# Performance work log

Measured on AMD Instinct MI355X. Metric: run time of the kernel, lower is better.

## Reference

```python
import jax, jax.numpy as jnp
import numpy as np

NP_, NA, NPR = 3000, 25, 1071
N = NP_ + NA + NPR          # 4096 total nodes
D = 256                     # latent_dim
H = 8                       # num_heads
DH = D // H                 # head dim 32
FF = 4 * D                  # feed-forward dim
BLOCKS = 3                  # args.block_num
E = 131072                  # edges = N * 32 avg degree
EPS = 1e-5


def setup_inputs() -> dict:
    key = jax.random.key(0)
    ks = jax.random.split(key, 16)
    s = 1.0 / np.sqrt(D)
    return {
        "adj_row": jax.random.randint(ks[0], (E,), 0, N, dtype=jnp.int32),
        "adj_col": jax.random.randint(ks[1], (E,), 0, N, dtype=jnp.int32),
        "adj_val": jax.random.uniform(ks[2], (E,), dtype=jnp.float32),
        "pe": jax.random.normal(ks[3], (NP_, D), dtype=jnp.float32) * s,
        "ae": jax.random.normal(ks[4], (NA, D), dtype=jnp.float32) * s,
        "qe": jax.random.normal(ks[5], (NPR, D), dtype=jnp.float32) * s,
        "Wqkv": jax.random.normal(ks[6], (D, 3 * D), dtype=jnp.float32) * s,
        "Wo": jax.random.normal(ks[7], (D, D), dtype=jnp.float32) * s,
        "W1": jax.random.normal(ks[8], (D, FF), dtype=jnp.float32) * s,
        "b1": jnp.zeros((FF,), dtype=jnp.float32),
        "W2": jax.random.normal(ks[9], (FF, D), dtype=jnp.float32) * (1.0 / np.sqrt(FF)),
        "b2": jnp.zeros((D,), dtype=jnp.float32),
        "ln1_g": jnp.ones((D,), dtype=jnp.float32),
        "ln1_b": jnp.zeros((D,), dtype=jnp.float32),
        "ln2_g": jnp.ones((D,), dtype=jnp.float32),
        "ln2_b": jnp.zeros((D,), dtype=jnp.float32),
    }


def _layer_norm(x, g, b):
    m = jnp.mean(x, axis=-1, keepdims=True)
    v = jnp.mean(jnp.square(x - m), axis=-1, keepdims=True)
    return (x - m) * jax.lax.rsqrt(v + EPS) * g + b


def _encoder_layer(x, Wqkv, Wo, W1, b1, W2, b2, ln1_g, ln1_b, ln2_g, ln2_b):
    # x: [N, D]; standard post-LN transformer encoder (dropout = 0)
    qkv = x @ Wqkv                                   # [N, 3D]
    q, k, v = jnp.split(qkv, 3, axis=-1)
    q = q.reshape(N, H, DH)
    k = k.reshape(N, H, DH)
    v = v.reshape(N, H, DH)
    scores = jnp.einsum("nhd,mhd->hnm", q, k) / np.sqrt(DH)  # [H, N, N]
    att = jax.nn.softmax(scores, axis=-1)
    o = jnp.einsum("hnm,mhd->nhd", att, v).reshape(N, D) @ Wo
    x = _layer_norm(x + o, ln1_g, ln1_b)
    h = jax.nn.relu(x @ W1 + b1) @ W2 + b2
    return _layer_norm(x + h, ln2_g, ln2_b)


def _spmm(adj_row, adj_col, adj_val, x):
    # sparse [N,N] @ dense [N,D] via gather + segment-sum scatter
    msgs = adj_val[:, None] * x[adj_col]             # [E, D]
    return jax.ops.segment_sum(msgs, adj_row, num_segments=N)


def reference(adj_row, adj_col, adj_val, pe, ae, qe, Wqkv, Wo, W1, b1, W2, b2,
              ln1_g, ln1_b, ln2_g, ln2_b):
    cur = jnp.concatenate([pe, ae, qe], axis=0)      # [N, D]
    total = cur
    for _ in range(BLOCKS):
        t = _spmm(adj_row, adj_col, adj_val, cur)
        t = _encoder_layer(t, Wqkv, Wo, W1, b1, W2, b2, ln1_g, ln1_b, ln2_g, ln2_b)
        cur = t + cur                                # residual per block
        total = total + cur                          # sum over embeds list
    protein = total[:NP_]
    aa = total[NP_:NP_ + NA]
    prop = total[NP_ + NA:]
    return total, protein, aa, prop
```

## Files before the change

### kernel.cpp

```cpp
#include <hip/hip_runtime.h>
#include <hip/hip_bf16.h>


#define NPROT 3000
#define NAA   25
#define NPROP 1071
#define NTOT  4096
#define DIM   256
#define NH    8
#define DHD   32
#define FFD   1024
#define NEDGE 131072
#define LNEPS 1e-5f
#define KSPLIT 4
#define KVQ (NTOT/KSPLIT)

typedef unsigned short u16;
typedef unsigned int u32;
typedef __attribute__((ext_vector_type(8))) short short8v;
typedef __attribute__((ext_vector_type(4))) float float4v;
typedef __attribute__((ext_vector_type(2))) unsigned int uint2v;

__device__ __forceinline__ u16 f2bu(float x){
  union { __hip_bfloat16 h; u16 u; } c; c.h = __float2bfloat16(x); return c.u;
}
__device__ __forceinline__ float bu2f(u16 u){
  union { u32 i; float f; } c; c.i = ((u32)u) << 16; return c.f;
}
__device__ __forceinline__ float4v mfma16(short8v a, short8v b, float4v c){
  return __builtin_amdgcn_mfma_f32_16x16x32_bf16(a, b, c, 0, 0, 0);
}
__device__ __forceinline__ u32 packbf(float lo, float hi){
  u32 ul = __builtin_bit_cast(u32, lo);
  u32 uh = __builtin_bit_cast(u32, hi);
  return (ul >> 16) | (uh & 0xFFFF0000u);
}

__global__ __launch_bounds__(256) void k_embed(const float* __restrict__ pe, const float* __restrict__ ae,
                                               const float* __restrict__ qe,
                                               float* __restrict__ cur, float* __restrict__ tot){
  int i = blockIdx.x*256 + threadIdx.x;
  int row = i >> 8;
  float v;
  if (row < NPROT)           v = pe[i];
  else if (row < NPROT+NAA)  v = ae[i - NPROT*DIM];
  else                       v = qe[i - (NPROT+NAA)*DIM];
  cur[i] = v; tot[i] = v;
}

__global__ __launch_bounds__(256) void k_zero(int* __restrict__ p, int n){
  int i = blockIdx.x*256 + threadIdx.x; if (i < n) p[i] = 0;
}

__global__ __launch_bounds__(256) void k_wconv(const float* __restrict__ W, u16* __restrict__ Wt,
                                               int K, int N){
  int n = blockIdx.x;
  for (int k = threadIdx.x; k < K; k += 256)
    Wt[(size_t)n*K + k] = f2bu(W[(size_t)k*N + n]);
}

__global__ __launch_bounds__(256) void k_hist(const int* __restrict__ rows, int* __restrict__ cnt){
  int e = blockIdx.x*256 + threadIdx.x; if (e < NEDGE) atomicAdd(&cnt[rows[e]], 1);
}

__global__ __launch_bounds__(64) void k_scan(const int* __restrict__ cnt, int* __restrict__ rowptr,
                                             int* __restrict__ cursor){
  int lane = threadIdx.x;
  int sum = 0;
  for (int i = 0; i < 64; ++i) sum += cnt[lane*64 + i];
  int pref = sum;
  #pragma unroll
  for (int off = 1; off < 64; off <<= 1){
    int u = __shfl_up(pref, off);
    if (lane >= off) pref += u;
  }
  int run = pref - sum;
  for (int i = 0; i < 64; ++i){
    int c = cnt[lane*64 + i];
    rowptr[lane*64 + i] = run;
    cursor[lane*64 + i] = run;
    run += c;
  }
  if (lane == 63) rowptr[NTOT] = run;
}

__global__ __launch_bounds__(256) void k_scatter(const int* __restrict__ rows, const int* __restrict__ cols,
                                                 const float* __restrict__ vals, int* __restrict__ cursor,
                                                 int* __restrict__ ccol, float* __restrict__ cval){
  int e = blockIdx.x*256 + threadIdx.x; if (e >= NEDGE) return;
  int p = atomicAdd(&cursor[rows[e]], 1);
  ccol[p] = cols[e]; cval[p] = vals[e];
}

__global__ __launch_bounds__(256) void k_spmm(const int* __restrict__ rowptr, const int* __restrict__ ccol,
                                              const float* __restrict__ cval, const float* __restrict__ x,
                                              float* __restrict__ out, u16* __restrict__ outb){
  int r = blockIdx.x, c = threadIdx.x;
  int s = rowptr[r], e = rowptr[r+1];
  float acc = 0.f;
  for (int i = s; i < e; ++i)
    acc += cval[i] * x[((size_t)ccol[i] << 8) + c];
  out[((size_t)r << 8) + c] = acc;
  outb[((size_t)r << 8) + c] = f2bu(acc);
}

template<int RELU, int BIAS, int BF16OUT>
__global__ __launch_bounds__(256) void k_gemm64(const u16* __restrict__ A, const u16* __restrict__ Wt,
                                                const float* __restrict__ bias, void* __restrict__ Cv,
                                                int M, int K, int Nc){
  __shared__ u16 Al[64*64];
  __shared__ u16 Bl[64*64];
  const int tid = threadIdx.x;
  const int w  = tid >> 6, l = tid & 63, lr = l & 15, g = l >> 4;
  const int row0 = blockIdx.y*64, col0 = blockIdx.x*64;
  const int wm = (w >> 1)*32, wn = (w & 1)*32;
  const int sm = tid >> 2;
  const int so = (tid & 3)*2;
  float4v acc[2][2] = {};

  for (int k0 = 0; k0 < K; k0 += 64){
    const u16* As = A  + (size_t)(row0 + sm)*K + k0 + so*8;
    const u16* Bs = Wt + (size_t)(col0 + sm)*K + k0 + so*8;
    #pragma unroll
    for (int j = 0; j < 2; ++j){
      int o = so + j;
      int slot = o ^ (sm & 7);
      *(short8v*)(Al + sm*64 + slot*8) = *(const short8v*)(As + j*8);
      *(short8v*)(Bl + sm*64 + slot*8) = *(const short8v*)(Bs + j*8);
    }
    __syncthreads();
    #pragma unroll
    for (int kk = 0; kk < 2; ++kk){
      short8v af[2], bfr[2];
      #pragma unroll
      for (int i = 0; i < 2; ++i){
        int am = wm + 16*i + lr;
        af[i]  = *(const short8v*)(Al + am*64 + (((4*kk + g) ^ (am & 7))*8));
        int bn = wn + 16*i + lr;
        bfr[i] = *(const short8v*)(Bl + bn*64 + (((4*kk + g) ^ (bn & 7))*8));
      }
      acc[0][0] = mfma16(af[0], bfr[0], acc[0][0]);
      acc[0][1] = mfma16(af[0], bfr[1], acc[0][1]);
      acc[1][0] = mfma16(af[1], bfr[0], acc[1][0]);
      acc[1][1] = mfma16(af[1], bfr[1], acc[1][1]);
    }
    __syncthreads();
  }

  #pragma unroll
  for (int mi = 0; mi < 2; ++mi){
    #pragma unroll
    for (int ni = 0; ni < 2; ++ni){
      int col = col0 + wn + 16*ni + lr;
      float bv = BIAS ? bias[col] : 0.f;
      #pragma unroll
      for (int j = 0; j < 4; ++j){
        int row = row0 + wm + 16*mi + 4*g + j;
        float v = acc[mi][ni][j] + bv;
        if (RELU) v = fmaxf(v, 0.f);
        if (BF16OUT) ((u16*)Cv)[(size_t)row*Nc + col] = f2bu(v);
        else         ((float*)Cv)[(size_t)row*Nc + col] = v;
      }
    }
  }
}

__global__ __launch_bounds__(256) void k_attn_mfma(const u16* __restrict__ qbf,
                                                   u16* __restrict__ op,
                                                   float* __restrict__ mbuf, float* __restrict__ lbuf){
  __shared__ u16 Vt[2][32*64];
  __shared__ u16 Pl[4][16*64];
  __shared__ float Fl[4][16];
  const int h   = blockIdx.y;
  const int ks  = blockIdx.z;
  const int qb  = blockIdx.x * 64;
  const int tid = threadIdx.x;
  const int w   = tid >> 6;
  const int l   = tid & 63;
  const int lr  = l & 15;
  const int g   = l >> 4;
  const int sr  = tid >> 2;
  const int sq  = tid & 3;
  const float SC  = 0.17677669529663687f;
  const float SCL = 0.25503837f;
  u16* opart = op + (size_t)ks*NTOT*DIM;

  short8v qf = *(const short8v*)(qbf + (size_t)(qb + 16*w + lr)*768 + h*DHD + 8*g);
  short8v ones;
  #pragma unroll
  for (int j = 0; j < 8; ++j) ones[j] = (short)0x3F80;

  float4v oa0 = {0.f,0.f,0.f,0.f}, oa1 = {0.f,0.f,0.f,0.f};
  float4v accl = {0.f,0.f,0.f,0.f};
  float mrun = -1e30f;
  u16* pw = &Pl[w][0];

  const u16* vp = qbf + (size_t)(ks*KVQ + sr)*768 + 512 + h*DHD + 8*sq;
  const u16* kp = qbf + (size_t)(ks*KVQ + lr)*768 + 256 + h*DHD + 8*g;
  short8v vreg = *(const short8v*)vp;
  short8v kf0 = *(const short8v*)(kp);
  short8v kf1 = *(const short8v*)(kp + (size_t)16*768);
  short8v kf2 = *(const short8v*)(kp + (size_t)32*768);
  short8v kf3 = *(const short8v*)(kp + (size_t)48*768);

  const int NIT = KVQ/64;
  for (int t = 0; t < NIT; ++t){
    u16* vt = &Vt[t & 1][0];
    #pragma unroll
    for (int j = 0; j < 8; ++j){
      int row  = 8*sq + j;
      int slot = (sr >> 3) ^ j;
      vt[row*64 + slot*8 + (sr & 7)] = (u16)vreg[j];
    }
    __syncthreads();
    vp += (size_t)64*768;
    if (t + 1 < NIT) vreg = *(const short8v*)vp;

    float4v s0 = mfma16(kf0, qf, (float4v){0.f,0.f,0.f,0.f});
    float4v s1 = mfma16(kf1, qf, (float4v){0.f,0.f,0.f,0.f});
    float4v s2 = mfma16(kf2, qf, (float4v){0.f,0.f,0.f,0.f});
    float4v s3 = mfma16(kf3, qf, (float4v){0.f,0.f,0.f,0.f});
    if (t + 1 < NIT){
      const u16* kn = kp + (size_t)(t+1)*64*768;
      kf0 = *(const short8v*)(kn);
      kf1 = *(const short8v*)(kn + (size_t)16*768);
      kf2 = *(const short8v*)(kn + (size_t)32*768);
      kf3 = *(const short8v*)(kn + (size_t)48*768);
    }

    float m0 = fmaxf(fmaxf(fmaxf(s0[0],s0[1]),s0[2]),s0[3]);
    float m1 = fmaxf(fmaxf(fmaxf(s1[0],s1[1]),s1[2]),s1[3]);
    float m2 = fmaxf(fmaxf(fmaxf(s2[0],s2[1]),s2[2]),s2[3]);
    float m3 = fmaxf(fmaxf(fmaxf(s3[0],s3[1]),s3[2]),s3[3]);
    float tm = fmaxf(fmaxf(fmaxf(m0,m1),m2),m3);
    tm = fmaxf(tm, __shfl_xor(tm, 16));
    tm = fmaxf(tm, __shfl_xor(tm, 32));
    const bool nomax = __all(tm <= mrun);
    float fac = 1.f;
    if (!nomax){
      float mn = fmaxf(mrun, tm);
      fac = exp2f((mrun - mn)*SCL);
      mrun = mn;
    }
    float mns = mrun*SCL;
    #pragma unroll
    for (int j = 0; j < 4; ++j){
      s0[j] = exp2f(__builtin_fmaf(s0[j], SCL, -mns));
      s1[j] = exp2f(__builtin_fmaf(s1[j], SCL, -mns));
      s2[j] = exp2f(__builtin_fmaf(s2[j], SCL, -mns));
      s3[j] = exp2f(__builtin_fmaf(s3[j], SCL, -mns));
    }

    {
      int gh = g >> 1, gl = 4*(g & 1);
      uint2v* d0 = (uint2v*)(pw + lr*64 + ((0 + gh) ^ (lr & 7))*8 + gl);
      uint2v* d1 = (uint2v*)(pw + lr*64 + ((2 + gh) ^ (lr & 7))*8 + gl);
      uint2v* d2 = (uint2v*)(pw + lr*64 + ((4 + gh) ^ (lr & 7))*8 + gl);
      uint2v* d3 = (uint2v*)(pw + lr*64 + ((6 + gh) ^ (lr & 7))*8 + gl);
      *d0 = (uint2v){packbf(s0[0],s0[1]), packbf(s0[2],s0[3])};
      *d1 = (uint2v){packbf(s1[0],s1[1]), packbf(s1[2],s1[3])};
      *d2 = (uint2v){packbf(s2[0],s2[1]), packbf(s2[2],s2[3])};
      *d3 = (uint2v){packbf(s3[0],s3[1]), packbf(s3[2],s3[3])};
    }

    if (!nomax){
      if (g == 0) Fl[w][lr] = fac;
      float fq0 = Fl[w][4*g+0], fq1 = Fl[w][4*g+1], fq2 = Fl[w][4*g+2], fq3 = Fl[w][4*g+3];
      oa0[0]*=fq0; oa0[1]*=fq1; oa0[2]*=fq2; oa0[3]*=fq3;
      oa1[0]*=fq0; oa1[1]*=fq1; oa1[2]*=fq2; oa1[3]*=fq3;
      accl[0]*=fq0; accl[1]*=fq1; accl[2]*=fq2; accl[3]*=fq3;
    }

    #pragma unroll
    for (int kk = 0; kk < 2; ++kk){
      int slotp = (4*kk + g) ^ (lr & 7);
      short8v pa = *(const short8v*)(pw + lr*64 + slotp*8);
      short8v v0 = *(const short8v*)(vt + lr*64        + slotp*8);
      short8v v1 = *(const short8v*)(vt + (lr+16)*64   + slotp*8);
      oa0  = mfma16(pa, v0, oa0);
      oa1  = mfma16(pa, v1, oa1);
      accl = mfma16(pa, ones, accl);
    }
  }

  #pragma unroll
  for (int j = 0; j < 4; ++j){
    size_t row = (size_t)(qb + 16*w + 4*g + j);
    opart[row*DIM + h*DHD + lr]      = f2bu(oa0[j]);
    opart[row*DIM + h*DHD + 16 + lr] = f2bu(oa1[j]);
  }
  if (l < 16){
    size_t mi = (size_t)(ks*NH + h)*NTOT + qb + 16*w + lr;
    mbuf[mi] = mrun*SC;
  }
  if (lr == 0){
    #pragma unroll
    for (int j = 0; j < 4; ++j){
      size_t mi = (size_t)(ks*NH + h)*NTOT + qb + 16*w + 4*g + j;
      lbuf[mi] = accl[j];
    }
  }
}

__global__ __launch_bounds__(256) void k_attn_merge(const u16* __restrict__ op,
                                                    const float* __restrict__ mbuf, const float* __restrict__ lbuf,
                                                    u16* __restrict__ obf){
  int i = blockIdx.x*256 + threadIdx.x;
  int r = i >> 8, c = i & 255, h = c >> 5;
  float m[KSPLIT], wgt[KSPLIT];
  float M = -1e30f;
  #pragma unroll
  for (int k = 0; k < KSPLIT; ++k){
    m[k] = mbuf[(size_t)(k*NH + h)*NTOT + r];
    M = fmaxf(M, m[k]);
  }
  float L = 0.f, acc = 0.f;
  #pragma unroll
  for (int k = 0; k < KSPLIT; ++k){
    wgt[k] = __expf(m[k] - M);
    L   += wgt[k]*lbuf[(size_t)(k*NH + h)*NTOT + r];
    acc += wgt[k]*bu2f(op[(size_t)k*NTOT*DIM + i]);
  }
  obf[i] = f2bu(acc / L);
}

template<int DUAL>
__global__ __launch_bounds__(256) void k_add_ln(const float* __restrict__ a, const float* __restrict__ b,
                                                const float* __restrict__ g, const float* __restrict__ be,
                                                float* __restrict__ out, u16* __restrict__ out2){
  __shared__ float red[4];
  int r = blockIdx.x, c = threadIdx.x;
  float v = a[((size_t)r << 8) + c] + b[((size_t)r << 8) + c];
  float s = v;
  #pragma unroll
  for (int off = 32; off; off >>= 1) s += __shfl_down(s, off);
  if ((c & 63) == 0) red[c >> 6] = s;
  __syncthreads();
  float mean = (red[0]+red[1]+red[2]+red[3]) * (1.f/DIM);
  __syncthreads();
  float d = v - mean;
  float s2 = d*d;
  #pragma unroll
  for (int off = 32; off; off >>= 1) s2 += __shfl_down(s2, off);
  if ((c & 63) == 0) red[c >> 6] = s2;
  __syncthreads();
  float var = (red[0]+red[1]+red[2]+red[3]) * (1.f/DIM);
  float rv = d * rsqrtf(var + LNEPS) * g[c] + be[c];
  out[((size_t)r << 8) + c] = rv;
  if (DUAL) out2[((size_t)r << 8) + c] = f2bu(rv);
}

__global__ __launch_bounds__(256) void k_add_ln_upd(const float* __restrict__ a, const float* __restrict__ b,
                                                    const float* __restrict__ g, const float* __restrict__ be,
                                                    float* __restrict__ cur, float* __restrict__ tot){
  __shared__ float red[4];
  int r = blockIdx.x, c = threadIdx.x;
  size_t idx = ((size_t)r << 8) + c;
  float v = a[idx] + b[idx];
  float s = v;
  #pragma unroll
  for (int off = 32; off; off >>= 1) s += __shfl_down(s, off);
  if ((c & 63) == 0) red[c >> 6] = s;
  __syncthreads();
  float mean = (red[0]+red[1]+red[2]+red[3]) * (1.f/DIM);
  __syncthreads();
  float d = v - mean;
  float s2 = d*d;
  #pragma unroll
  for (int off = 32; off; off >>= 1) s2 += __shfl_down(s2, off);
  if ((c & 63) == 0) red[c >> 6] = s2;
  __syncthreads();
  float var = (red[0]+red[1]+red[2]+red[3]) * (1.f/DIM);
  float rv = d * rsqrtf(var + LNEPS) * g[c] + be[c];
  float cu = cur[idx] + rv;
  cur[idx] = cu;
  tot[idx] += cu;
}

__global__ __launch_bounds__(256) void k_out(const float* __restrict__ tot, float* __restrict__ out){
  int i = blockIdx.x*256 + threadIdx.x;
  float v = tot[i];
  out[i] = v;
  out[NTOT*DIM + i] = v;
}

extern "C" void kernel_launch(void* const* d_in, const int* in_sizes, int n_in,
                              void* d_out, int out_size, void* d_ws, size_t ws_size,
                              hipStream_t stream){
  const int*   adj_row = (const int*)  d_in[0];
  const int*   adj_col = (const int*)  d_in[1];
  const float* adj_val = (const float*)d_in[2];
  const float* pe   = (const float*)d_in[3];
  const float* ae   = (const float*)d_in[4];
  const float* qe   = (const float*)d_in[5];
  const float* Wqkv = (const float*)d_in[6];
  const float* Wo   = (const float*)d_in[7];
  const float* W1   = (const float*)d_in[8];
  const float* b1   = (const float*)d_in[9];
  const float* W2   = (const float*)d_in[10];
  const float* b2   = (const float*)d_in[11];
  const float* g1   = (const float*)d_in[12];
  const float* be1  = (const float*)d_in[13];
  const float* g2   = (const float*)d_in[14];
  const float* be2  = (const float*)d_in[15];
  float* out = (float*)d_out;

  char* w = (char*)d_ws;
  float* cur  = (float*)w; w += (size_t)NTOT*DIM*4;
  float* tot  = (float*)w; w += (size_t)NTOT*DIM*4;
  float* tf   = (float*)w; w += (size_t)NTOT*DIM*4;
  float* pbuf = (float*)w; w += (size_t)NTOT*DIM*4;
  float* x1   = (float*)w; w += (size_t)NTOT*DIM*4;
  u16* tbf    = (u16*)w;   w += (size_t)NTOT*DIM*2;
  u16* obf    = (u16*)w;   w += (size_t)NTOT*DIM*2;
  u16* x1b    = (u16*)w;   w += (size_t)NTOT*DIM*2;
  u16* hq     = (u16*)w;   w += (size_t)NTOT*FFD*2;
  u16* wqkvt  = (u16*)w;   w += (size_t)768*256*2;
  u16* wot    = (u16*)w;   w += (size_t)256*256*2;
  u16* w1t    = (u16*)w;   w += (size_t)1024*256*2;
  u16* w2t    = (u16*)w;   w += (size_t)256*1024*2;
  int* rowptr = (int*)w;   w += (size_t)(NTOT+1)*4;
  int* cnt    = (int*)w;   w += (size_t)NTOT*4;
  int* cursor = (int*)w;   w += (size_t)NTOT*4;
  int* ccol   = (int*)w;   w += (size_t)NEDGE*4;
  float* cval = (float*)w; w += (size_t)NEDGE*4;
  u16* qbf  = hq;
  u16* opbf = (u16*)pbuf;
  float* mbuf = (float*)tbf;
  float* lbuf = mbuf + (size_t)KSPLIT*NH*NTOT;

  k_zero<<<16, 256, 0, stream>>>(cnt, NTOT);
  k_embed<<<NTOT, 256, 0, stream>>>(pe, ae, qe, cur, tot);
  k_hist<<<NEDGE/256, 256, 0, stream>>>(adj_row, cnt);
  k_scan<<<1, 64, 0, stream>>>(cnt, rowptr, cursor);
  k_scatter<<<NEDGE/256, 256, 0, stream>>>(adj_row, adj_col, adj_val, cursor, ccol, cval);
  k_wconv<<<768,  256, 0, stream>>>(Wqkv, wqkvt, 256, 768);
  k_wconv<<<256,  256, 0, stream>>>(Wo,   wot,   256, 256);
  k_wconv<<<1024, 256, 0, stream>>>(W1,   w1t,   256, 1024);
  k_wconv<<<256,  256, 0, stream>>>(W2,   w2t,  1024, 256);

  for (int blk = 0; blk < 3; ++blk){
    k_spmm<<<NTOT, 256, 0, stream>>>(rowptr, ccol, cval, cur, tf, tbf);
    k_gemm64<0,0,1><<<dim3(768/64, NTOT/64), 256, 0, stream>>>(tbf, wqkvt, nullptr, qbf, NTOT, 256, 768);
    k_attn_mfma<<<dim3(NTOT/64, NH, KSPLIT), 256, 0, stream>>>(qbf, opbf, mbuf, lbuf);
    k_attn_merge<<<NTOT*DIM/256, 256, 0, stream>>>(opbf, mbuf, lbuf, obf);
    k_gemm64<0,0,0><<<dim3(256/64, NTOT/64), 256, 0, stream>>>(obf, wot, nullptr, pbuf, NTOT, 256, 256);
    k_add_ln<1><<<NTOT, 256, 0, stream>>>(tf, pbuf, g1, be1, x1, x1b);
    k_gemm64<1,1,1><<<dim3(1024/64, NTOT/64), 256, 0, stream>>>(x1b, w1t, b1, hq, NTOT, 256, 1024);
    k_gemm64<0,1,0><<<dim3(256/64, NTOT/64), 256, 0, stream>>>(hq, w2t, b2, pbuf, NTOT, 1024, 256);
    k_add_ln_upd<<<NTOT, 256, 0, stream>>>(x1, pbuf, g2, be2, cur, tot);
  }
  k_out<<<NTOT, 256, 0, stream>>>(tot, out);
}
```

Before: 492.5 us.

## Process 128 keys per attention iteration and halve the KV split

The flash-attention kernel now consumes 128 keys per loop iteration: eight K fragments, two transposed V tiles and a 128-wide P tile. The KV split drops from 4 to 2, so fewer partial outputs have to be combined afterwards. The rescale factor is broadcast with wave shuffles instead of a shared-memory round trip. The aim is fewer barriers and loop overheads and more MFMA/exp work per iteration, at the cost of more registers and half as many blocks. The prefetch of the next K/V tile is now unconditional, so the last iteration reads past the end of the slice.

```diff
diff --git a/kernel.cpp b/kernel.cpp
--- a/kernel.cpp
+++ b/kernel.cpp
@@ -12,7 +12,7 @@
 #define FFD   1024
 #define NEDGE 131072
 #define LNEPS 1e-5f
-#define KSPLIT 4
+#define KSPLIT 2
 #define KVQ (NTOT/KSPLIT)
 
 typedef unsigned short u16;
@@ -168,9 +168,8 @@
 __global__ __launch_bounds__(256) void k_attn_mfma(const u16* __restrict__ qbf,
                                                    u16* __restrict__ op,
                                                    float* __restrict__ mbuf, float* __restrict__ lbuf){
-  __shared__ u16 Vt[2][32*64];
-  __shared__ u16 Pl[4][16*64];
-  __shared__ float Fl[4][16];
+  __shared__ u16 Vt[2][2][32*64];
+  __shared__ u16 Pl[4][16*128];
   const int h   = blockIdx.y;
   const int ks  = blockIdx.z;
   const int qb  = blockIdx.x * 64;
@@ -197,42 +196,42 @@
 
   const u16* vp = qbf + (size_t)(ks*KVQ + sr)*768 + 512 + h*DHD + 8*sq;
   const u16* kp = qbf + (size_t)(ks*KVQ + lr)*768 + 256 + h*DHD + 8*g;
-  short8v vreg = *(const short8v*)vp;
-  short8v kf0 = *(const short8v*)(kp);
-  short8v kf1 = *(const short8v*)(kp + (size_t)16*768);
-  short8v kf2 = *(const short8v*)(kp + (size_t)32*768);
-  short8v kf3 = *(const short8v*)(kp + (size_t)48*768);
-
-  const int NIT = KVQ/64;
+  short8v vrA = *(const short8v*)vp;
+  short8v vrB = *(const short8v*)(vp + (size_t)64*768);
+  short8v kf[8];
+  #pragma unroll
+  for (int i = 0; i < 8; ++i) kf[i] = *(const short8v*)(kp + (size_t)16*i*768);
+
+  const int NIT = KVQ/128;
   for (int t = 0; t < NIT; ++t){
-    u16* vt = &Vt[t & 1][0];
+    u16* vt0 = &Vt[t & 1][0][0];
+    u16* vt1 = &Vt[t & 1][1][0];
     #pragma unroll
     for (int j = 0; j < 8; ++j){
       int row  = 8*sq + j;
       int slot = (sr >> 3) ^ j;
-      vt[row*64 + slot*8 + (sr & 7)] = (u16)vreg[j];
+      vt0[row*64 + slot*8 + (sr & 7)] = (u16)vrA[j];
+      vt1[row*64 + slot*8 + (sr & 7)] = (u16)vrB[j];
     }
     __syncthreads();
-    vp += (size_t)64*768;
-    if (t + 1 < NIT) vreg = *(const short8v*)vp;
-
-    float4v s0 = mfma16(kf0, qf, (float4v){0.f,0.f,0.f,0.f});
-    float4v s1 = mfma16(kf1, qf, (float4v){0.f,0.f,0.f,0.f});
-    float4v s2 = mfma16(kf2, qf, (float4v){0.f,0.f,0.f,0.f});
-    float4v s3 = mfma16(kf3, qf, (float4v){0.f,0.f,0.f,0.f});
-    if (t + 1 < NIT){
-      const u16* kn = kp + (size_t)(t+1)*64*768;
-      kf0 = *(const short8v*)(kn);
-      kf1 = *(const short8v*)(kn + (size_t)16*768);
-      kf2 = *(const short8v*)(kn + (size_t)32*768);
-      kf3 = *(const short8v*)(kn + (size_t)48*768);
-    }
-
-    float m0 = fmaxf(fmaxf(fmaxf(s0[0],s0[1]),s0[2]),s0[3]);
-    float m1 = fmaxf(fmaxf(fmaxf(s1[0],s1[1]),s1[2]),s1[3]);
-    float m2 = fmaxf(fmaxf(fmaxf(s2[0],s2[1]),s2[2]),s2[3]);
-    float m3 = fmaxf(fmaxf(fmaxf(s3[0],s3[1]),s3[2]),s3[3]);
-    float tm = fmaxf(fmaxf(fmaxf(m0,m1),m2),m3);
+    vp += (size_t)128*768;
+    vrA = *(const short8v*)vp;
+    vrB = *(const short8v*)(vp + (size_t)64*768);
+
+    float4v s[8];
+    #pragma unroll
+    for (int i = 0; i < 8; ++i)
+      s[i] = mfma16(kf[i], qf, (float4v){0.f,0.f,0.f,0.f});
+    kp += (size_t)128*768;
+    #pragma unroll
+    for (int i = 0; i < 8; ++i) kf[i] = *(const short8v*)(kp + (size_t)16*i*768);
+
+    float pm[8];
+    #pragma unroll
+    for (int i = 0; i < 8; ++i)
+      pm[i] = fmaxf(fmaxf(fmaxf(s[i][0],s[i][1]),s[i][2]),s[i][3]);
+    float tm = fmaxf(fmaxf(fmaxf(pm[0],pm[1]),fmaxf(pm[2],pm[3])),
+                     fmaxf(fmaxf(pm[4],pm[5]),fmaxf(pm[6],pm[7])));
     tm = fmaxf(tm, __shfl_xor(tm, 16));
     tm = fmaxf(tm, __shfl_xor(tm, 32));
     const bool nomax = __all(tm <= mrun);
@@ -244,39 +243,41 @@
     }
     float mns = mrun*SCL;
     #pragma unroll
-    for (int j = 0; j < 4; ++j){
-      s0[j] = exp2f(__builtin_fmaf(s0[j], SCL, -mns));
-      s1[j] = exp2f(__builtin_fmaf(s1[j], SCL, -mns));
-      s2[j] = exp2f(__builtin_fmaf(s2[j], SCL, -mns));
-      s3[j] = exp2f(__builtin_fmaf(s3[j], SCL, -mns));
+    for (int i = 0; i < 8; ++i){
+      s[i][0] = exp2f(__builtin_fmaf(s[i][0], SCL, -mns));
+      s[i][1] = exp2f(__builtin_fmaf(s[i][1], SCL, -mns));
+      s[i][2] = exp2f(__builtin_fmaf(s[i][2], SCL, -mns));
+      s[i][3] = exp2f(__builtin_fmaf(s[i][3], SCL, -mns));
     }
 
     {
       int gh = g >> 1, gl = 4*(g & 1);
-      uint2v* d0 = (uint2v*)(pw + lr*64 + ((0 + gh) ^ (lr & 7))*8 + gl);
-      uint2v* d1 = (uint2v*)(pw + lr*64 + ((2 + gh) ^ (lr & 7))*8 + gl);
-      uint2v* d2 = (uint2v*)(pw + lr*64 + ((4 + gh) ^ (lr & 7))*8 + gl);
-      uint2v* d3 = (uint2v*)(pw + lr*64 + ((6 + gh) ^ (lr & 7))*8 + gl);
-      *d0 = (uint2v){packbf(s0[0],s0[1]), packbf(s0[2],s0[3])};
-      *d1 = (uint2v){packbf(s1[0],s1[1]), packbf(s1[2],s1[3])};
-      *d2 = (uint2v){packbf(s2[0],s2[1]), packbf(s2[2],s2[3])};
-      *d3 = (uint2v){packbf(s3[0],s3[1]), packbf(s3[2],s3[3])};
+      #pragma unroll
+      for (int i = 0; i < 8; ++i){
+        int o = 2*i + gh;
+        uint2v* d = (uint2v*)(pw + lr*128 + ((o ^ lr)*8) + gl);
+        *d = (uint2v){packbf(s[i][0], s[i][1]), packbf(s[i][2], s[i][3])};
+      }
     }
 
     if (!nomax){
-      if (g == 0) Fl[w][lr] = fac;
-      float fq0 = Fl[w][4*g+0], fq1 = Fl[w][4*g+1], fq2 = Fl[w][4*g+2], fq3 = Fl[w][4*g+3];
+      float fq0 = __shfl(fac, 4*g + 0);
+      float fq1 = __shfl(fac, 4*g + 1);
+      float fq2 = __shfl(fac, 4*g + 2);
+      float fq3 = __shfl(fac, 4*g + 3);
       oa0[0]*=fq0; oa0[1]*=fq1; oa0[2]*=fq2; oa0[3]*=fq3;
       oa1[0]*=fq0; oa1[1]*=fq1; oa1[2]*=fq2; oa1[3]*=fq3;
       accl[0]*=fq0; accl[1]*=fq1; accl[2]*=fq2; accl[3]*=fq3;
     }
 
     #pragma unroll
-    for (int kk = 0; kk < 2; ++kk){
-      int slotp = (4*kk + g) ^ (lr & 7);
-      short8v pa = *(const short8v*)(pw + lr*64 + slotp*8);
-      short8v v0 = *(const short8v*)(vt + lr*64        + slotp*8);
-      short8v v1 = *(const short8v*)(vt + (lr+16)*64   + slotp*8);
+    for (int kk = 0; kk < 4; ++kk){
+      int op8 = (4*kk + g) ^ lr;
+      short8v pa = *(const short8v*)(pw + lr*128 + op8*8);
+      const u16* vt = (kk < 2) ? vt0 : vt1;
+      int slotv = (4*(kk & 1) + g) ^ (lr & 7);
+      short8v v0 = *(const short8v*)(vt + lr*64        + slotv*8);
+      short8v v1 = *(const short8v*)(vt + (lr+16)*64   + slotv*8);
       oa0  = mfma16(pa, v0, oa0);
       oa1  = mfma16(pa, v1, oa1);
       accl = mfma16(pa, ones, accl);
```

Result: no change. 499.9 us (+1.5%).
